# Performance work log

Measured on AMD Instinct MI355X. Metric: run time of the kernel, lower is better.

## Reference

```python
import jax, jax.numpy as jnp
import numpy as np

DIM = 1024
HEADS = 8
DIM_HEAD = 64
INNER = HEADS * DIM_HEAD  # 512
B, N = 2, 2048
SCALE = DIM_HEAD ** -0.5
EPS = 1e-5


def layer_norm(x, gamma):
    # lucidrains LayerNorm: learned gamma, fixed zero beta
    mu = jnp.mean(x, axis=-1, keepdims=True)
    var = jnp.var(x, axis=-1, keepdims=True)
    return (x - mu) * jax.lax.rsqrt(var + EPS) * gamma


def setup_inputs() -> dict:
    key = jax.random.key(0)
    ks = jax.random.split(key, 8)
    x = jax.random.normal(ks[0], (B, N, DIM), dtype=jnp.float32)
    mask = jax.random.randint(ks[1], (B, N), 0, 2) > 0  # bool padding mask
    attn_bias = jax.random.normal(ks[2], (HEADS, N, N), dtype=jnp.float32)
    gamma = jnp.ones((DIM,), dtype=jnp.float32)
    s = 0.02
    Wq = jax.random.normal(ks[3], (DIM, INNER), dtype=jnp.float32) * s
    Wkv = jax.random.normal(ks[4], (DIM, 2 * DIM_HEAD), dtype=jnp.float32) * s
    Wo = jax.random.normal(ks[5], (INNER, DIM), dtype=jnp.float32) * s
    return {"x": x, "mask": mask, "attn_bias": attn_bias, "gamma": gamma,
            "Wq": Wq, "Wkv": Wkv, "Wo": Wo}


def reference(x, mask, attn_bias, gamma, Wq, Wkv, Wo):
    b, n, _ = x.shape
    kv_input = x  # NOTE: K/V use the UN-normalized input (per source ordering)
    xn = layer_norm(x, gamma)
    q = xn @ Wq                       # [b, n, inner]
    kv = kv_input @ Wkv               # [b, n, 2*dh]
    k, v = jnp.split(kv, 2, axis=-1)  # each [b, n, dh] (single shared KV head)
    q = q.reshape(b, n, HEADS, DIM_HEAD).transpose(0, 2, 1, 3) * SCALE  # [b,h,n,dh]
    sim = jnp.einsum('bhid,bjd->bhij', q, k)
    sim = sim + attn_bias             # attn_bias [h,i,j] broadcasts over batch
    neg = -jnp.finfo(sim.dtype).max
    sim = jnp.where(mask[:, None, None, :], sim, neg)
    causal_mask = jnp.triu(jnp.ones((n, n), dtype=bool), k=1)
    sim = jnp.where(causal_mask, neg, sim)
    attn = jax.nn.softmax(sim, axis=-1)
    out = jnp.einsum('bhij,bjd->bhid', attn, v)          # [b,h,n,dh]
    out = out.transpose(0, 2, 1, 3).reshape(b, n, INNER)  # [b,n,inner]
    return out @ Wo
```

## Files before the change

kernel.cpp:

```cpp
#include <hip/hip_runtime.h>
#include <cfloat>
#include <cstdint>
#include <cstddef>

#define N_TOK 2048
#define D_MODEL 1024
#define N_HEAD 8
#define D_HEAD 64
#define N_BATCH 2
#define INNER_DIM 512

typedef __attribute__((ext_vector_type(4))) float f32x4;
typedef __bf16 bfv8 __attribute__((ext_vector_type(8)));

__device__ __forceinline__ short f2bf(float f) {
  union { float f; unsigned u; } x{f};
  unsigned r = (x.u + 0x7fffu + ((x.u >> 16) & 1u)) >> 16;
  return (short)r;
}
__device__ __forceinline__ float bf2f(short s) {
  union { unsigned u; float f; } x;
  x.u = ((unsigned)(unsigned short)s) << 16;
  return x.f;
}
__device__ __forceinline__ void gload_lds16(const void* g, void* l) {
  __builtin_amdgcn_global_load_lds(
      (const __attribute__((address_space(1))) void*)g,
      (__attribute__((address_space(3))) void*)l, 16, 0, 0);
}

__global__ __launch_bounds__(256) void ln_cast_kernel(
    const float* __restrict__ x, const float* __restrict__ gamma,
    short* __restrict__ xn, short* __restrict__ xb) {
  const int row = blockIdx.x;
  const int tid = threadIdx.x;
  const float4 v = ((const float4*)(x + (size_t)row * D_MODEL))[tid];
  float s = v.x + v.y + v.z + v.w;
  float s2 = v.x * v.x + v.y * v.y + v.z * v.z + v.w * v.w;
#pragma unroll
  for (int off = 1; off < 64; off <<= 1) {
    s += __shfl_xor(s, off);
    s2 += __shfl_xor(s2, off);
  }
  __shared__ float red[8];
  const int wid = tid >> 6;
  if ((tid & 63) == 0) { red[wid] = s; red[wid + 4] = s2; }
  __syncthreads();
  s = red[0] + red[1] + red[2] + red[3];
  s2 = red[4] + red[5] + red[6] + red[7];
  const float mu = s * (1.f / D_MODEL);
  const float var = s2 * (1.f / D_MODEL) - mu * mu;
  const float rstd = rsqrtf(var + 1e-5f);
  const float4 g = ((const float4*)gamma)[tid];
  short4 xnv, xbv;
  xnv.x = f2bf((v.x - mu) * rstd * g.x);
  xnv.y = f2bf((v.y - mu) * rstd * g.y);
  xnv.z = f2bf((v.z - mu) * rstd * g.z);
  xnv.w = f2bf((v.w - mu) * rstd * g.w);
  xbv.x = f2bf(v.x); xbv.y = f2bf(v.y); xbv.z = f2bf(v.z); xbv.w = f2bf(v.w);
  ((short4*)(xn + (size_t)row * D_MODEL))[tid] = xnv;
  ((short4*)(xb + (size_t)row * D_MODEL))[tid] = xbv;
}

__global__ __launch_bounds__(256) void wcast_t_kernel(
    const float* __restrict__ W, short* __restrict__ Wt, int K, int Nc) {
  __shared__ short t[64][65];
  const int n0 = blockIdx.x * 64, k0 = blockIdx.y * 64;
  const int tid = threadIdx.x;
#pragma unroll
  for (int i = 0; i < 16; ++i) {
    int lin = i * 256 + tid;
    int kr = lin >> 6, nc = lin & 63;
    t[nc][kr] = f2bf(W[(size_t)(k0 + kr) * Nc + n0 + nc]);
  }
  __syncthreads();
#pragma unroll
  for (int i = 0; i < 16; ++i) {
    int lin = i * 256 + tid;
    int nr = lin >> 6, kc = lin & 63;
    Wt[(size_t)(n0 + nr) * K + k0 + kc] = t[nr][kc];
  }
}

template <int EPI>
__global__ __launch_bounds__(256) void gemm_nt_kernel(
    const short* __restrict__ A, const short* __restrict__ Bt,
    void* __restrict__ C0, void* __restrict__ C1, int M, int N, int K) {
  __shared__ __align__(16) short As[128 * 64];
  __shared__ __align__(16) short Bs[128 * 64];
  const int tid = threadIdx.x;
  const int lane = tid & 63, wid = tid >> 6;
  const int l15 = lane & 15, l4 = lane >> 4;
  const int m0 = blockIdx.y * 128, n0 = blockIdx.x * 128;
  const int wr = (wid >> 1) * 64, wc = (wid & 1) * 64;
  f32x4 acc[4][4] = {};
  for (int k0 = 0; k0 < K; k0 += 64) {
#pragma unroll
    for (int it = 0; it < 4; ++it) {
      int c = it * 256 + tid;
      int r = c >> 3, cc = (c & 7) << 3;
      gload_lds16(A + (size_t)(m0 + r) * K + k0 + cc, As + (size_t)(it * 256 + wid * 64) * 8);
      gload_lds16(Bt + (size_t)(n0 + r) * K + k0 + cc, Bs + (size_t)(it * 256 + wid * 64) * 8);
    }
    __syncthreads();
#pragma unroll
    for (int kk = 0; kk < 2; ++kk) {
      bfv8 af[4], bfr[4];
#pragma unroll
      for (int i = 0; i < 4; ++i) {
        af[i] = *(const bfv8*)&As[(wr + i * 16 + l15) * 64 + kk * 32 + l4 * 8];
        bfr[i] = *(const bfv8*)&Bs[(wc + i * 16 + l15) * 64 + kk * 32 + l4 * 8];
      }
#pragma unroll
      for (int mi = 0; mi < 4; ++mi)
#pragma unroll
        for (int ni = 0; ni < 4; ++ni)
          acc[mi][ni] = __builtin_amdgcn_mfma_f32_16x16x32_bf16(af[mi], bfr[ni], acc[mi][ni], 0, 0, 0);
    }
    __syncthreads();
  }
#pragma unroll
  for (int mi = 0; mi < 4; ++mi) {
#pragma unroll
    for (int ni = 0; ni < 4; ++ni) {
#pragma unroll
      for (int r = 0; r < 4; ++r) {
        const int row = m0 + wr + mi * 16 + l4 * 4 + r;
        const int col = n0 + wc + ni * 16 + l15;
        const float v = acc[mi][ni][r];
        if (EPI == 0) {
          const int b = row >> 11, n = row & (N_TOK - 1);
          const int h = col >> 6, d = col & 63;
          ((short*)C0)[(((size_t)(b * N_HEAD + h)) * N_TOK + n) * D_HEAD + d] = f2bf(v * 0.125f);
        } else if (EPI == 1) {
          const int b = row >> 11, n = row & (N_TOK - 1);
          if (col < 64)
            ((short*)C0)[((size_t)b * N_TOK + n) * D_HEAD + col] = f2bf(v);
          else
            ((short*)C1)[((size_t)b * D_HEAD + (col - 64)) * N_TOK + n] = f2bf(v);
        } else {
          ((float*)C0)[(size_t)row * D_MODEL + col] = v;
        }
      }
    }
  }
}

__global__ __launch_bounds__(256) void vmean_kernel(const short* __restrict__ vt,
                                                    float* __restrict__ vm) {
  const int bd = blockIdx.x;
  const short* rowp = vt + (size_t)bd * N_TOK;
  const int tid = threadIdx.x;
  float s = 0.f;
  for (int i = tid; i < N_TOK; i += 256) s += bf2f(rowp[i]);
#pragma unroll
  for (int off = 1; off < 64; off <<= 1) s += __shfl_xor(s, off);
  __shared__ float red[4];
  if ((tid & 63) == 0) red[tid >> 6] = s;
  __syncthreads();
  if (tid == 0) vm[bd] = (red[0] + red[1] + red[2] + red[3]) * (1.f / N_TOK);
}

__global__ __launch_bounds__(64, 2) void attn_kernel(
    const short* __restrict__ qg,
    const short* __restrict__ kg,
    const short* __restrict__ vtg,
    const float* __restrict__ bias,
    const int* __restrict__ mask,
    const float* __restrict__ vm,
    short* __restrict__ og) {
  const int bh = blockIdx.x;
  const int qw = 127 - (int)blockIdx.y;
  const int b = bh >> 3, h = bh & 7;
  const int lane = threadIdx.x;
  const int l15 = lane & 15, l4 = lane >> 4;

  __shared__ __align__(16) short plds[1024];

  const int qrow0 = qw * 16;
  const short* qp = qg + ((size_t)bh * N_TOK + qrow0 + l15) * D_HEAD + l4 * 8;
  const bfv8 qf0 = *(const bfv8*)qp;
  const bfv8 qf1 = *(const bfv8*)(qp + 32);
  const int i_base = qrow0 + l4 * 4;
  const int nt = qw / 8 + 1;

  f32x4 oacc[4] = {};
  float m_r[4], l_r[4];
#pragma unroll
  for (int r = 0; r < 4; ++r) { m_r[r] = -FLT_MAX; l_r[r] = 0.f; }

  const float* bias_base = bias + ((size_t)h * N_TOK + i_base) * N_TOK + l15;
  const int* mask_b = mask + b * N_TOK + l15;

  float bX[32], bY[32];
#pragma unroll
  for (int mf = 0; mf < 8; ++mf)
#pragma unroll
    for (int r = 0; r < 4; ++r)
      bX[mf * 4 + r] = bias_base[(size_t)r * N_TOK + mf * 16];

  int t = 0;
#define BODY(BC, BN)                                                                    \
  {                                                                                     \
    const int j0 = t * 128;                                                             \
                          \
    int mk[8];                                                                          \
    _Pragma("unroll") for (int mf = 0; mf < 8; ++mf) mk[mf] = mask_b[j0 + mf * 16];     \
    bfv8 vf[16];                                                                        \
    const short* vp = vtg + ((size_t)b * D_HEAD + l15) * N_TOK + j0 + l4 * 8;           \
    _Pragma("unroll") for (int hh = 0; hh < 2; ++hh)                                    \
        _Pragma("unroll") for (int ks = 0; ks < 2; ++ks)                                \
            _Pragma("unroll") for (int df = 0; df < 4; ++df)                            \
                vf[hh * 8 + ks * 4 + df] =                                              \
                    *(const bfv8*)(vp + hh * 64 + df * (16 * N_TOK) + ks * 32);         \
    f32x4 s[8] = {};                                                                    \
    const short* kp = kg + ((size_t)b * N_TOK + j0 + l15) * D_HEAD + l4 * 8;            \
    _Pragma("unroll") for (int ks = 0; ks < 2; ++ks) {                                  \
      const bfv8 qf = ks ? qf1 : qf0;                                                   \
      _Pragma("unroll") for (int mf = 0; mf < 8; ++mf) {                                \
        const bfv8 kf = *(const bfv8*)(kp + mf * (16 * D_HEAD) + ks * 32);              \
        s[mf] = __builtin_amdgcn_mfma_f32_16x16x32_bf16(qf, kf, s[mf], 0, 0, 0);        \
      }                                                                                 \
    }                                                                                   \
    __builtin_amdgcn_sched_barrier(0);                                                  \
          \
    {                                                                                   \
      const int jn = (t + 1 < nt) ? (t + 1) * 128 : j0;                                 \
      _Pragma("unroll") for (int mf = 0; mf < 8; ++mf)                                  \
          _Pragma("unroll") for (int r = 0; r < 4; ++r)                                 \
              BN[mf * 4 + r] = bias_base[(size_t)r * N_TOK + jn + mf * 16];             \
    }                                                                                   \
    __builtin_amdgcn_sched_barrier(0);                                                  \
    float rowmax[4] = {-FLT_MAX, -FLT_MAX, -FLT_MAX, -FLT_MAX};                         \
    _Pragma("unroll") for (int mf = 0; mf < 8; ++mf) {                                  \
      const int j = j0 + mf * 16 + l15;                                                 \
      _Pragma("unroll") for (int r = 0; r < 4; ++r) {                                   \
        float v = s[mf][r] + BC[mf * 4 + r];                                            \
        const bool ok = (j <= i_base + r) && (mk[mf] != 0);                             \
        v = ok ? v : -FLT_MAX;                                                          \
        s[mf][r] = v;                                                                   \
        rowmax[r] = fmaxf(rowmax[r], v);                                                \
      }                                                                                 \
    }                                                                                   \
    _Pragma("unroll") for (int off = 1; off < 16; off <<= 1)                            \
        _Pragma("unroll") for (int r = 0; r < 4; ++r)                                   \
            rowmax[r] = fmaxf(rowmax[r], __shfl_xor(rowmax[r], off));                   \
    float alpha[4], rsum[4];                                                            \
    _Pragma("unroll") for (int r = 0; r < 4; ++r) {                                     \
      const float mn = fmaxf(m_r[r], rowmax[r]);                                        \
      alpha[r] = __expf(m_r[r] - mn);                                                   \
      m_r[r] = mn;                                                                      \
      float rs = 0.f;                                                                   \
      _Pragma("unroll") for (int mf = 0; mf < 8; ++mf) {                                \
        const float e = __expf(s[mf][r] - mn);                                          \
        s[mf][r] = e;                                                                   \
        rs += e;                                                                        \
      }                                                                                 \
      rsum[r] = rs;                                                                     \
    }                                                                                   \
    _Pragma("unroll") for (int off = 1; off < 16; off <<= 1)                            \
        _Pragma("unroll") for (int r = 0; r < 4; ++r)                                   \
            rsum[r] += __shfl_xor(rsum[r], off);                                        \
    _Pragma("unroll") for (int r = 0; r < 4; ++r)                                       \
        l_r[r] = l_r[r] * alpha[r] + rsum[r];                                           \
    _Pragma("unroll") for (int df = 0; df < 4; ++df)                                    \
        _Pragma("unroll") for (int r = 0; r < 4; ++r)                                   \
            oacc[df][r] *= alpha[r];                                                    \
    _Pragma("unroll") for (int hh = 0; hh < 2; ++hh) {                                  \
      _Pragma("unroll") for (int nf = 0; nf < 4; ++nf) {                                \
        const int ch = (nf * 16 + l15) >> 3;                                            \
        const int cl = l15 & 7;                                                         \
        _Pragma("unroll") for (int r = 0; r < 4; ++r) {                                 \
          const int row = l4 * 4 + r;                                                   \
          const int g = row * 8 + (ch ^ (row & 7));                                     \
          plds[g * 8 + cl] = f2bf(s[hh * 4 + nf][r]);                                   \
        }                                                                               \
      }                                                                                 \
      _Pragma("unroll") for (int ks = 0; ks < 2; ++ks) {                                \
        const int g = l15 * 8 + ((ks * 4 + l4) ^ (l15 & 7));                            \
        const bfv8 pf = *(const bfv8*)&plds[g * 8];                                     \
        _Pragma("unroll") for (int df = 0; df < 4; ++df)                                \
          oacc[df] = __builtin_amdgcn_mfma_f32_16x16x32_bf16(                           \
              pf, vf[hh * 8 + ks * 4 + df], oacc[df], 0, 0, 0);                         \
      }                                                                                 \
    }                                                                                   \
    ++t;                                                                                \
  }

  while (t < nt) {
    BODY(bX, bY)
    if (t >= nt) break;
    BODY(bY, bX)
  }
#undef BODY

#pragma unroll
  for (int r = 0; r < 4; ++r) {
    const int i = i_base + r;
    const bool degen = (m_r[r] == -FLT_MAX);
    const float sc = degen ? 0.f : 1.f / l_r[r];
#pragma unroll
    for (int df = 0; df < 4; ++df) {
      const int d = df * 16 + l15;
      float v = oacc[df][r] * sc;
      if (degen) v = vm[b * D_HEAD + d];
      og[((size_t)b * N_TOK + i) * INNER_DIM + h * D_HEAD + d] = f2bf(v);
    }
  }
}

extern "C" void kernel_launch(void* const* d_in, const int* in_sizes, int n_in,
                              void* d_out, int out_size, void* d_ws, size_t ws_size,
                              hipStream_t stream) {
  const float* x = (const float*)d_in[0];
  const int* mask = (const int*)d_in[1];
  const float* bias = (const float*)d_in[2];
  const float* gamma = (const float*)d_in[3];
  const float* Wq = (const float*)d_in[4];
  const float* Wkv = (const float*)d_in[5];
  const float* Wo = (const float*)d_in[6];
  float* out = (float*)d_out;

  char* w = (char*)d_ws;
  short* xn = (short*)w;  w += (size_t)4096 * 1024 * 2;
  short* xb = (short*)w;  w += (size_t)4096 * 1024 * 2;
  short* wqt = (short*)w; w += (size_t)512 * 1024 * 2;
  short* wkvt = (short*)w; w += (size_t)128 * 1024 * 2;
  short* wot = (short*)w; w += (size_t)1024 * 512 * 2;
  short* q = (short*)w;   w += (size_t)16 * 2048 * 64 * 2;
  short* kb = (short*)w;  w += (size_t)2 * 2048 * 64 * 2;
  short* vt = (short*)w;  w += (size_t)2 * 64 * 2048 * 2;
  short* og = (short*)w;  w += (size_t)4096 * 512 * 2;
  float* vm = (float*)w;  w += 128 * 4;

  ln_cast_kernel<<<4096, 256, 0, stream>>>(x, gamma, xn, xb);
  wcast_t_kernel<<<dim3(8, 16), 256, 0, stream>>>(Wq, wqt, 1024, 512);
  wcast_t_kernel<<<dim3(2, 16), 256, 0, stream>>>(Wkv, wkvt, 1024, 128);
  wcast_t_kernel<<<dim3(16, 8), 256, 0, stream>>>(Wo, wot, 512, 1024);
  gemm_nt_kernel<0><<<dim3(4, 32), 256, 0, stream>>>(xn, wqt, q, nullptr, 4096, 512, 1024);
  gemm_nt_kernel<1><<<dim3(1, 32), 256, 0, stream>>>(xb, wkvt, kb, vt, 4096, 128, 1024);
  vmean_kernel<<<128, 256, 0, stream>>>(vt, vm);
  attn_kernel<<<dim3(16, 128), 64, 0, stream>>>(q, kb, vt, bias, mask, vm, og);
  gemm_nt_kernel<2><<<dim3(8, 32), 256, 0, stream>>>(og, wot, out, nullptr, 4096, 1024, 512);
}
```

Before: 165.2 us.

## Merge weight casts into one launch and fuse Q/KV GEMMs with smaller tiles

The three weight cast-transpose launches become one kernel that dispatches on block index. The separate Q and KV projection GEMMs become a single launch over a 10x32 grid with 128x64 tiles, so the 128-column KV GEMM no longer runs alone on only 32 blocks. This cuts launch count and improves occupancy on the small GEMM. In exchange the Q GEMM now uses smaller tiles, which lowers data reuse per block.

```diff
diff --git a/kernel.cpp b/kernel.cpp
--- a/kernel.cpp
+++ b/kernel.cpp
@@ -62,10 +62,25 @@
   ((short4*)(xb + (size_t)row * D_MODEL))[tid] = xbv;
 }
 
-__global__ __launch_bounds__(256) void wcast_t_kernel(
-    const float* __restrict__ W, short* __restrict__ Wt, int K, int Nc) {
+__global__ __launch_bounds__(256) void wcast_all_kernel(
+    const float* __restrict__ Wq, const float* __restrict__ Wkv,
+    const float* __restrict__ Wo, short* __restrict__ wqt,
+    short* __restrict__ wkvt, short* __restrict__ wot) {
+  const int bid = blockIdx.x;
+  const float* W; short* Wt; int K, Nc, n0, k0;
+  if (bid < 128) {
+    W = Wq; Wt = wqt; K = 1024; Nc = 512;
+    n0 = (bid & 7) * 64; k0 = (bid >> 3) * 64;
+  } else if (bid < 160) {
+    const int t = bid - 128;
+    W = Wkv; Wt = wkvt; K = 1024; Nc = 128;
+    n0 = (t & 1) * 64; k0 = (t >> 1) * 64;
+  } else {
+    const int t = bid - 160;
+    W = Wo; Wt = wot; K = 512; Nc = 1024;
+    n0 = (t & 15) * 64; k0 = (t >> 4) * 64;
+  }
   __shared__ short t[64][65];
-  const int n0 = blockIdx.x * 64, k0 = blockIdx.y * 64;
   const int tid = threadIdx.x;
 #pragma unroll
   for (int i = 0; i < 16; ++i) {
@@ -82,10 +97,81 @@
   }
 }
 
-template <int EPI>
-__global__ __launch_bounds__(256) void gemm_nt_kernel(
+__global__ __launch_bounds__(256) void qkv_gemm_kernel(
+    const short* __restrict__ xn, const short* __restrict__ xb,
+    const short* __restrict__ wqt, const short* __restrict__ wkvt,
+    short* __restrict__ q, short* __restrict__ kb, short* __restrict__ vt) {
+  const bool isQ = blockIdx.x < 8;
+  const short* A = isQ ? xn : xb;
+  const short* Bt = isQ ? wqt : wkvt;
+  const int n0 = (isQ ? blockIdx.x : (blockIdx.x - 8)) * 64;
+  const int m0 = blockIdx.y * 128;
+  const int K = 1024;
+  __shared__ __align__(16) short As[128 * 64];
+  __shared__ __align__(16) short Bs[64 * 64];
+  const int tid = threadIdx.x;
+  const int lane = tid & 63, wid = tid >> 6;
+  const int l15 = lane & 15, l4 = lane >> 4;
+  const int wr = wid * 32;
+  f32x4 acc[2][4] = {};
+  for (int k0 = 0; k0 < K; k0 += 64) {
+#pragma unroll
+    for (int it = 0; it < 4; ++it) {
+      int c = it * 256 + tid;
+      int r = c >> 3, cc = (c & 7) << 3;
+      gload_lds16(A + (size_t)(m0 + r) * K + k0 + cc, As + (size_t)(it * 256 + wid * 64) * 8);
+    }
+#pragma unroll
+    for (int it = 0; it < 2; ++it) {
+      int c = it * 256 + tid;
+      int r = c >> 3, cc = (c & 7) << 3;
+      gload_lds16(Bt + (size_t)(n0 + r) * K + k0 + cc, Bs + (size_t)(it * 256 + wid * 64) * 8);
+    }
+    __syncthreads();
+#pragma unroll
+    for (int kk = 0; kk < 2; ++kk) {
+      bfv8 af[2], bfr[4];
+#pragma unroll
+      for (int i = 0; i < 2; ++i)
+        af[i] = *(const bfv8*)&As[(wr + i * 16 + l15) * 64 + kk * 32 + l4 * 8];
+#pragma unroll
+      for (int i = 0; i < 4; ++i)
+        bfr[i] = *(const bfv8*)&Bs[(i * 16 + l15) * 64 + kk * 32 + l4 * 8];
+#pragma unroll
+      for (int mi = 0; mi < 2; ++mi)
+#pragma unroll
+        for (int ni = 0; ni < 4; ++ni)
+          acc[mi][ni] = __builtin_amdgcn_mfma_f32_16x16x32_bf16(af[mi], bfr[ni], acc[mi][ni], 0, 0, 0);
+    }
+    __syncthreads();
+  }
+#pragma unroll
+  for (int mi = 0; mi < 2; ++mi) {
+#pragma unroll
+    for (int ni = 0; ni < 4; ++ni) {
+#pragma unroll
+      for (int r = 0; r < 4; ++r) {
+        const int row = m0 + wr + mi * 16 + l4 * 4 + r;
+        const int col = n0 + ni * 16 + l15;
+        const float v = acc[mi][ni][r];
+        const int b = row >> 11, n = row & (N_TOK - 1);
+        if (isQ) {
+          const int h = col >> 6, d = col & 63;
+          q[(((size_t)(b * N_HEAD + h)) * N_TOK + n) * D_HEAD + d] = f2bf(v * 0.125f);
+        } else {
+          if (col < 64)
+            kb[((size_t)b * N_TOK + n) * D_HEAD + col] = f2bf(v);
+          else
+            vt[((size_t)b * D_HEAD + (col - 64)) * N_TOK + n] = f2bf(v);
+        }
+      }
+    }
+  }
+}
+
+__global__ __launch_bounds__(256) void ogemm_kernel(
     const short* __restrict__ A, const short* __restrict__ Bt,
-    void* __restrict__ C0, void* __restrict__ C1, int M, int N, int K) {
+    float* __restrict__ C, int M, int N, int K) {
   __shared__ __align__(16) short As[128 * 64];
   __shared__ __align__(16) short Bs[128 * 64];
   const int tid = threadIdx.x;
@@ -120,30 +206,15 @@
     __syncthreads();
   }
 #pragma unroll
-  for (int mi = 0; mi < 4; ++mi) {
-#pragma unroll
-    for (int ni = 0; ni < 4; ++ni) {
+  for (int mi = 0; mi < 4; ++mi)
+#pragma unroll
+    for (int ni = 0; ni < 4; ++ni)
 #pragma unroll
       for (int r = 0; r < 4; ++r) {
         const int row = m0 + wr + mi * 16 + l4 * 4 + r;
         const int col = n0 + wc + ni * 16 + l15;
-        const float v = acc[mi][ni][r];
-        if (EPI == 0) {
-          const int b = row >> 11, n = row & (N_TOK - 1);
-          const int h = col >> 6, d = col & 63;
-          ((short*)C0)[(((size_t)(b * N_HEAD + h)) * N_TOK + n) * D_HEAD + d] = f2bf(v * 0.125f);
-        } else if (EPI == 1) {
-          const int b = row >> 11, n = row & (N_TOK - 1);
-          if (col < 64)
-            ((short*)C0)[((size_t)b * N_TOK + n) * D_HEAD + col] = f2bf(v);
-          else
-            ((short*)C1)[((size_t)b * D_HEAD + (col - 64)) * N_TOK + n] = f2bf(v);
-        } else {
-          ((float*)C0)[(size_t)row * D_MODEL + col] = v;
-        }
+        C[(size_t)row * N + col] = acc[mi][ni][r];
       }
-    }
-  }
 }
 
 __global__ __launch_bounds__(256) void vmean_kernel(const short* __restrict__ vt,
@@ -203,7 +274,6 @@
 #define BODY(BC, BN)                                                                    \
   {                                                                                     \
     const int j0 = t * 128;                                                             \
-                          \
     int mk[8];                                                                          \
     _Pragma("unroll") for (int mf = 0; mf < 8; ++mf) mk[mf] = mask_b[j0 + mf * 16];     \
     bfv8 vf[16];                                                                        \
@@ -223,7 +293,6 @@
       }                                                                                 \
     }                                                                                   \
     __builtin_amdgcn_sched_barrier(0);                                                  \
-          \
     {                                                                                   \
       const int jn = (t + 1 < nt) ? (t + 1) * 128 : j0;                                 \
       _Pragma("unroll") for (int mf = 0; mf < 8; ++mf)                                  \
@@ -334,12 +403,9 @@
   float* vm = (float*)w;  w += 128 * 4;
 
   ln_cast_kernel<<<4096, 256, 0, stream>>>(x, gamma, xn, xb);
-  wcast_t_kernel<<<dim3(8, 16), 256, 0, stream>>>(Wq, wqt, 1024, 512);
-  wcast_t_kernel<<<dim3(2, 16), 256, 0, stream>>>(Wkv, wkvt, 1024, 128);
-  wcast_t_kernel<<<dim3(16, 8), 256, 0, stream>>>(Wo, wot, 512, 1024);
-  gemm_nt_kernel<0><<<dim3(4, 32), 256, 0, stream>>>(xn, wqt, q, nullptr, 4096, 512, 1024);
-  gemm_nt_kernel<1><<<dim3(1, 32), 256, 0, stream>>>(xb, wkvt, kb, vt, 4096, 128, 1024);
+  wcast_all_kernel<<<288, 256, 0, stream>>>(Wq, Wkv, Wo, wqt, wkvt, wot);
+  qkv_gemm_kernel<<<dim3(10, 32), 256, 0, stream>>>(xn, xb, wqt, wkvt, q, kb, vt);
   vmean_kernel<<<128, 256, 0, stream>>>(vt, vm);
   attn_kernel<<<dim3(16, 128), 64, 0, stream>>>(q, kb, vt, bias, mask, vm, og);
-  gemm_nt_kernel<2><<<dim3(8, 32), 256, 0, stream>>>(og, wot, out, nullptr, 4096, 1024, 512);
-}
+  ogemm_kernel<<<dim3(8, 32), 256, 0, stream>>>(og, wot, out, 4096, 1024, 512);
+}
```

Measured after the change: 137.1 us. 17.0% less time.
